# Optimization experiments

Hardware: AMD Instinct MI355X
Metric: run time of the kernel (lower is better)

The kernel has to match this reference:

```python
import jax, jax.numpy as jnp
import numpy as np

NOOBJ_LAMBDA = 0.5
COORD_LAMBDA = 5.0


def _cxcywh_to_xyxy(b):
    cx, cy, w, h = b[..., 0], b[..., 1], b[..., 2], b[..., 3]
    return jnp.stack([cx - w / 2, cy - h / 2, cx + w / 2, cy + h / 2], axis=-1)


def _pairwise_iou(a, b):
    # a: [B, N, 4] xyxy (preds), b: [B, M, 4] xyxy (targets) -> [B, N, M]
    lt = jnp.maximum(a[:, :, None, :2], b[:, None, :, :2])
    rb = jnp.minimum(a[:, :, None, 2:], b[:, None, :, 2:])
    wh = jnp.clip(rb - lt, 0.0)
    inter = wh[..., 0] * wh[..., 1]
    area_a = (a[..., 2] - a[..., 0]) * (a[..., 3] - a[..., 1])
    area_b = (b[..., 2] - b[..., 0]) * (b[..., 3] - b[..., 1])
    union = area_a[:, :, None] + area_b[:, None, :] - inter
    return inter / jnp.where(union > 0, union, 1.0)


def setup_inputs() -> dict:
    key = jax.random.key(0)
    kp, kt, km = jax.random.split(key, 3)
    B = 8192
    # positive values so sqrt(w), sqrt(h) is well-defined (as the torch code assumes)
    pred = jax.random.uniform(kp, (B, 7, 7, 30), dtype=jnp.float32, minval=0.05, maxval=1.0)
    target = jax.random.uniform(kt, (B, 7, 7, 30), dtype=jnp.float32, minval=0.05, maxval=1.0)
    # target confidence channel (index 4) is the obj/noobj indicator: 0 or 1
    obj = (jax.random.uniform(km, (B, 7, 7)) < 0.2).astype(jnp.float32)
    target = target.at[..., 4].set(obj)
    return {"pred_tensor": pred, "target_tensor": target}


def reference(pred_tensor, target_tensor):
    B = pred_tensor.shape[0]
    pred = pred_tensor.reshape(B, 49, 30)
    target = target_tensor.reshape(B, 49, 30)

    conf_t = target[..., 4]            # [B,49]
    noobj = conf_t == 0                # [B,49]
    obj = conf_t > 0                   # [B,49]

    # --- no-object confidence loss (channels 4 and 9) ---
    d4 = pred[..., 4] - target[..., 4]
    d9 = pred[..., 9] - target[..., 9]
    noobj_loss = jnp.sum(jnp.where(noobj, d4 * d4 + d9 * d9, 0.0))

    # --- object cells: 2 boxes per cell, padded to all 49 cells with a mask ---
    pb = pred[..., :10].reshape(B, 98, 5)
    tb = target[..., :10].reshape(B, 98, 5)
    box_mask = jnp.repeat(obj, 2, axis=1)  # [B,98]

    p_xyxy = _cxcywh_to_xyxy(pb[..., :4])
    t_xyxy = _cxcywh_to_xyxy(tb[..., :4])
    iou = _pairwise_iou(p_xyxy, t_xyxy)  # [B,98,98]
    pair_mask = box_mask[:, :, None] & box_mask[:, None, :]
    iou = jnp.where(pair_mask, iou, 0.0)
    max_iou = jnp.max(iou, axis=1)       # max over pred boxes, per target box [B,98]
    cmask = (max_iou != 0) & box_mask    # [B,98]

    cm = cmask.astype(pred.dtype)
    # coord (cx,cy) loss
    dxy = pb[..., :2] - tb[..., :2]
    coord_loss_cxcy = jnp.sum(cm * jnp.sum(dxy * dxy, axis=-1))
    # coord (sqrt w, sqrt h) loss
    dwh = jnp.sqrt(pb[..., 2:4]) - jnp.sqrt(tb[..., 2:4])
    coord_loss_wh = jnp.sum(cm * jnp.sum(dwh * dwh, axis=-1))
    # object confidence loss
    dconf = pb[..., 4] - tb[..., 4]
    obj_loss = jnp.sum(cm * dconf * dconf)

    # --- class loss over object cells ---
    dcls = pred[..., 10:] - target[..., 10:]
    cls_loss = jnp.sum(obj.astype(pred.dtype) * jnp.sum(dcls * dcls, axis=-1))

    bsz = jnp.asarray(B, pred.dtype)
    batch_cls_loss = cls_loss / bsz
    batch_obj_loss = (obj_loss + noobj_loss * NOOBJ_LAMBDA) / bsz
    batch_coord_loss = (coord_loss_cxcy + coord_loss_wh) * COORD_LAMBDA / bsz
    batch_loss = batch_cls_loss + batch_obj_loss + batch_coord_loss
    return (batch_loss, batch_cls_loss, batch_obj_loss, batch_coord_loss)
```

## Files before the change

kernel.cpp:

```cpp
#include <hip/hip_runtime.h>

#define CH 30
#define CELLS 49
#define ROW 1470
#define RPB 4
#define NPAIR 735
#define ITS 12

__device__ __forceinline__ float waveReduce(float v) {
    #pragma unroll
    for (int o = 32; o > 0; o >>= 1) v += __shfl_xor(v, o, 64);
    return v;
}

__global__ __launch_bounds__(256) void yolo_main(const float* __restrict__ pred,
                                                 const float* __restrict__ targ,
                                                 float* __restrict__ ws, int B) {
    const int w = threadIdx.x >> 6;
    const int lane = threadIdx.x & 63;
    const int r = blockIdx.x * RPB + w;
    if (r >= B) return;

    __shared__ float4 boxS[RPB][2 * CELLS];
    __shared__ int clist[RPB][CELLS];

    const float* P = pred + (size_t)r * ROW;
    const float* T = targ + (size_t)r * ROW;
    const float2* P2 = (const float2*)P;
    const float2* T2 = (const float2*)T;

    const int cl = lane < CELLS ? lane : CELLS - 1;
    const float conf = T[cl * CH + 4];

    float2 pv[ITS], tv[ITS];
    #pragma unroll
    for (int it = 0; it < ITS; ++it) {
        const int j = lane + it * 64;
        const int jc = j < NPAIR ? j : NPAIR - 1;
        pv[it] = P2[jc];
        tv[it] = T2[jc];
    }

    const bool isObj = (lane < CELLS) && (conf > 0.f);
    const unsigned long long mask = __ballot(isObj);
    const int nObj = __popcll(mask);
    if (isObj) clist[w][__popcll(mask & ((1ull << lane) - 1ull))] = lane;

    float cls = 0.f, objc = 0.f, coord = 0.f;
    #pragma unroll
    for (int it = 0; it < ITS; ++it) {
        const int j = lane + it * 64;
        const bool valid = j < NPAIR;
        const int cell = (j * 17477) >> 18;
        const int ch0 = 2 * (j - cell * 15);
        const float wobj = (float)((mask >> cell) & 1ull);
        const float dx = pv[it].x - tv[it].x;
        const float dy = pv[it].y - tv[it].y;
        cls += (valid && ch0 >= 10) ? wobj * (dx * dx + dy * dy) : 0.f;
        const float nn = (ch0 == 4 ? dx * dx : 0.f) + (ch0 == 8 ? dy * dy : 0.f);
        objc += valid ? 0.5f * (1.f - wobj) * nn : 0.f;
    }

    const int nBox = 2 * nObj;

    for (int e = lane; e < nBox; e += 64) {
        const int c = clist[w][e >> 1];
        const float* pb = P + c * CH + (e & 1) * 5;
        const float cx = pb[0], cy = pb[1], bw = pb[2], bh = pb[3];
        boxS[w][e] = make_float4(cx - 0.5f * bw, cy - 0.5f * bh,
                                 cx + 0.5f * bw, cy + 0.5f * bh);
    }

    for (int e = lane; e < nBox; e += 64) {
        const int c = clist[w][e >> 1];
        const float* tb = T + c * CH + (e & 1) * 5;
        const float tcx = tb[0], tcy = tb[1], tw = tb[2], th = tb[3];
        const float tx1 = tcx - 0.5f * tw, ty1 = tcy - 0.5f * th;
        const float tx2 = tcx + 0.5f * tw, ty2 = tcy + 0.5f * th;
        const float ta = (tx2 - tx1) * (ty2 - ty1);
        float maxiou = 0.f;
        for (int i = 0; i < nBox; ++i) {
            const float4 pb4 = boxS[w][i];
            const float lx = fmaxf(pb4.x, tx1), ly = fmaxf(pb4.y, ty1);
            const float rx = fminf(pb4.z, tx2), ry = fminf(pb4.w, ty2);
            const float iw = fmaxf(rx - lx, 0.f), ih = fmaxf(ry - ly, 0.f);
            const float inter = iw * ih;
            const float pa = (pb4.z - pb4.x) * (pb4.w - pb4.y);
            const float un = pa + ta - inter;
            const float iou = inter / (un > 0.f ? un : 1.f);
            maxiou = fmaxf(maxiou, iou);
        }
        if (maxiou != 0.f) {
            const float* pb = P + c * CH + (e & 1) * 5;
            const float dcx = pb[0] - tcx, dcy = pb[1] - tcy;
            coord += dcx * dcx + dcy * dcy;
            const float dw = sqrtf(pb[2]) - sqrtf(tw);
            const float dh = sqrtf(pb[3]) - sqrtf(th);
            coord += dw * dw + dh * dh;
            const float dc = pb[4] - tb[4];
            objc += dc * dc;
        }
    }

    cls = waveReduce(cls); objc = waveReduce(objc); coord = waveReduce(coord);
    if (lane == 0) {
        ws[r] = cls;
        ws[B + r] = objc;
        ws[2 * B + r] = coord;
    }
}

__global__ __launch_bounds__(1024) void yolo_reduce(const float* __restrict__ ws,
                                                    float* __restrict__ out,
                                                    int B, float invB) {
    const int tid = threadIdx.x;
    const int w = tid >> 6, lane = tid & 63;
    float c = 0.f, o = 0.f, x = 0.f;
    for (int i = tid; i < B; i += 1024) {
        c += ws[i];
        o += ws[B + i];
        x += ws[2 * B + i];
    }
    c = waveReduce(c); o = waveReduce(o); x = waveReduce(x);
    __shared__ float sred[16][3];
    if (lane == 0) { sred[w][0] = c; sred[w][1] = o; sred[w][2] = x; }
    __syncthreads();
    if (tid == 0) {
        float C = 0.f, O = 0.f, X = 0.f;
        #pragma unroll
        for (int k = 0; k < 16; ++k) { C += sred[k][0]; O += sred[k][1]; X += sred[k][2]; }
        const float bcls = C * invB;
        const float bobj = O * invB;
        const float bcoord = X * 5.0f * invB;
        out[0] = bcls + bobj + bcoord;
        out[1] = bcls;
        out[2] = bobj;
        out[3] = bcoord;
    }
}

extern "C" void kernel_launch(void* const* d_in, const int* in_sizes, int n_in,
                              void* d_out, int out_size, void* d_ws, size_t ws_size,
                              hipStream_t stream) {
    const float* pred = (const float*)d_in[0];
    const float* targ = (const float*)d_in[1];
    float* ws = (float*)d_ws;
    float* out = (float*)d_out;
    const int B = in_sizes[0] / ROW;
    const int NB = (B + RPB - 1) / RPB;

    yolo_main<<<NB, 256, 0, stream>>>(pred, targ, ws, B);
    yolo_reduce<<<1, 1024, 0, stream>>>(ws, out, B, 1.0f / (float)B);
}
```

Before: 122.0 us.

## Process two rows per wave and fuse final reduction via last-block atomic

Each wave now handles two batch rows, issuing the register loads for both rows up front so more memory requests are in flight per wave. The object mask is now built from the already-loaded target registers with a wave OR instead of a separate strided load. Per-block partial sums are combined in shared memory, and the last block to finish, found through an atomic counter, does the final reduction, which removes the second kernel launch. In exchange it doubles register use for the row buffers, adds a memset launch, and adds a thread fence and atomic per block.

```diff
diff --git a/kernel.cpp b/kernel.cpp
--- a/kernel.cpp
+++ b/kernel.cpp
@@ -3,9 +3,10 @@
 #define CH 30
 #define CELLS 49
 #define ROW 1470
-#define RPB 4
 #define NPAIR 735
 #define ITS 12
+#define RPW 2
+#define WPB 4
 
 __device__ __forceinline__ float waveReduce(float v) {
     #pragma unroll
@@ -13,40 +14,30 @@
     return v;
 }
 
-__global__ __launch_bounds__(256) void yolo_main(const float* __restrict__ pred,
-                                                 const float* __restrict__ targ,
-                                                 float* __restrict__ ws, int B) {
-    const int w = threadIdx.x >> 6;
-    const int lane = threadIdx.x & 63;
-    const int r = blockIdx.x * RPB + w;
-    if (r >= B) return;
-
-    __shared__ float4 boxS[RPB][2 * CELLS];
-    __shared__ int clist[RPB][CELLS];
-
-    const float* P = pred + (size_t)r * ROW;
-    const float* T = targ + (size_t)r * ROW;
-    const float2* P2 = (const float2*)P;
-    const float2* T2 = (const float2*)T;
-
-    const int cl = lane < CELLS ? lane : CELLS - 1;
-    const float conf = T[cl * CH + 4];
-
-    float2 pv[ITS], tv[ITS];
+__device__ __forceinline__ unsigned long long waveOr64(unsigned long long m) {
+    #pragma unroll
+    for (int o = 32; o > 0; o >>= 1) m |= __shfl_xor(m, o, 64);
+    return m;
+}
+
+__device__ __forceinline__ void processRow(const float* __restrict__ P,
+                                           const float* __restrict__ T,
+                                           const float2* pv, const float2* tv,
+                                           int lane, float4* boxS, int* clist,
+                                           float& cls, float& objc, float& coord) {
+    unsigned long long contrib = 0ull;
     #pragma unroll
     for (int it = 0; it < ITS; ++it) {
         const int j = lane + it * 64;
-        const int jc = j < NPAIR ? j : NPAIR - 1;
-        pv[it] = P2[jc];
-        tv[it] = T2[jc];
-    }
-
-    const bool isObj = (lane < CELLS) && (conf > 0.f);
-    const unsigned long long mask = __ballot(isObj);
+        const int cell = (j * 17477) >> 18;
+        const int rem = j - cell * 15;
+        if (j < NPAIR && rem == 2 && tv[it].x > 0.f) contrib |= (1ull << cell);
+    }
+    const unsigned long long mask = waveOr64(contrib);
     const int nObj = __popcll(mask);
-    if (isObj) clist[w][__popcll(mask & ((1ull << lane) - 1ull))] = lane;
-
-    float cls = 0.f, objc = 0.f, coord = 0.f;
+    const bool isObj = (lane < CELLS) && ((mask >> lane) & 1ull);
+    if (isObj) clist[__popcll(mask & ((1ull << lane) - 1ull))] = lane;
+
     #pragma unroll
     for (int it = 0; it < ITS; ++it) {
         const int j = lane + it * 64;
@@ -64,15 +55,15 @@
     const int nBox = 2 * nObj;
 
     for (int e = lane; e < nBox; e += 64) {
-        const int c = clist[w][e >> 1];
+        const int c = clist[e >> 1];
         const float* pb = P + c * CH + (e & 1) * 5;
         const float cx = pb[0], cy = pb[1], bw = pb[2], bh = pb[3];
-        boxS[w][e] = make_float4(cx - 0.5f * bw, cy - 0.5f * bh,
-                                 cx + 0.5f * bw, cy + 0.5f * bh);
+        boxS[e] = make_float4(cx - 0.5f * bw, cy - 0.5f * bh,
+                              cx + 0.5f * bw, cy + 0.5f * bh);
     }
 
     for (int e = lane; e < nBox; e += 64) {
-        const int c = clist[w][e >> 1];
+        const int c = clist[e >> 1];
         const float* tb = T + c * CH + (e & 1) * 5;
         const float tcx = tb[0], tcy = tb[1], tw = tb[2], th = tb[3];
         const float tx1 = tcx - 0.5f * tw, ty1 = tcy - 0.5f * th;
@@ -80,7 +71,7 @@
         const float ta = (tx2 - tx1) * (ty2 - ty1);
         float maxiou = 0.f;
         for (int i = 0; i < nBox; ++i) {
-            const float4 pb4 = boxS[w][i];
+            const float4 pb4 = boxS[i];
             const float lx = fmaxf(pb4.x, tx1), ly = fmaxf(pb4.y, ty1);
             const float rx = fminf(pb4.z, tx2), ry = fminf(pb4.w, ty2);
             const float iw = fmaxf(rx - lx, 0.f), ih = fmaxf(ry - ly, 0.f);
@@ -101,41 +92,98 @@
             objc += dc * dc;
         }
     }
+}
+
+__global__ __launch_bounds__(256) void yolo_main(const float* __restrict__ pred,
+                                                 const float* __restrict__ targ,
+                                                 float* __restrict__ ws,
+                                                 int* __restrict__ cnt,
+                                                 float* __restrict__ out,
+                                                 int B, float invB) {
+    const int w = threadIdx.x >> 6;
+    const int lane = threadIdx.x & 63;
+    const int NBLK = gridDim.x;
+    const int r0 = (blockIdx.x * WPB + w) * RPW;
+    const int r1 = r0 + 1;
+    const bool ok0 = r0 < B, ok1 = r1 < B;
+
+    __shared__ float4 boxS[WPB][2 * CELLS];
+    __shared__ int clist[WPB][CELLS];
+    __shared__ float sred[WPB][3];
+    __shared__ int lastFlag;
+
+    const float* P0 = pred + (size_t)r0 * ROW;
+    const float* T0 = targ + (size_t)r0 * ROW;
+    const float* P1 = pred + (size_t)r1 * ROW;
+    const float* T1 = targ + (size_t)r1 * ROW;
+
+    float2 pv0[ITS], tv0[ITS], pv1[ITS], tv1[ITS];
+    if (ok0) {
+        const float2* P2 = (const float2*)P0;
+        const float2* T2 = (const float2*)T0;
+        #pragma unroll
+        for (int it = 0; it < ITS; ++it) {
+            const int j = lane + it * 64;
+            const int jc = j < NPAIR ? j : NPAIR - 1;
+            pv0[it] = P2[jc];
+            tv0[it] = T2[jc];
+        }
+    }
+    if (ok1) {
+        const float2* P2 = (const float2*)P1;
+        const float2* T2 = (const float2*)T1;
+        #pragma unroll
+        for (int it = 0; it < ITS; ++it) {
+            const int j = lane + it * 64;
+            const int jc = j < NPAIR ? j : NPAIR - 1;
+            pv1[it] = P2[jc];
+            tv1[it] = T2[jc];
+        }
+    }
+
+    float cls = 0.f, objc = 0.f, coord = 0.f;
+    if (ok0) processRow(P0, T0, pv0, tv0, lane, boxS[w], clist[w], cls, objc, coord);
+    if (ok1) processRow(P1, T1, pv1, tv1, lane, boxS[w], clist[w], cls, objc, coord);
 
     cls = waveReduce(cls); objc = waveReduce(objc); coord = waveReduce(coord);
-    if (lane == 0) {
-        ws[r] = cls;
-        ws[B + r] = objc;
-        ws[2 * B + r] = coord;
-    }
-}
-
-__global__ __launch_bounds__(1024) void yolo_reduce(const float* __restrict__ ws,
-                                                    float* __restrict__ out,
-                                                    int B, float invB) {
-    const int tid = threadIdx.x;
-    const int w = tid >> 6, lane = tid & 63;
-    float c = 0.f, o = 0.f, x = 0.f;
-    for (int i = tid; i < B; i += 1024) {
-        c += ws[i];
-        o += ws[B + i];
-        x += ws[2 * B + i];
-    }
-    c = waveReduce(c); o = waveReduce(o); x = waveReduce(x);
-    __shared__ float sred[16][3];
-    if (lane == 0) { sred[w][0] = c; sred[w][1] = o; sred[w][2] = x; }
+    if (lane == 0) { sred[w][0] = cls; sred[w][1] = objc; sred[w][2] = coord; }
     __syncthreads();
-    if (tid == 0) {
-        float C = 0.f, O = 0.f, X = 0.f;
+    if (threadIdx.x == 0) {
+        float c = 0.f, o = 0.f, x = 0.f;
         #pragma unroll
-        for (int k = 0; k < 16; ++k) { C += sred[k][0]; O += sred[k][1]; X += sred[k][2]; }
-        const float bcls = C * invB;
-        const float bobj = O * invB;
-        const float bcoord = X * 5.0f * invB;
-        out[0] = bcls + bobj + bcoord;
-        out[1] = bcls;
-        out[2] = bobj;
-        out[3] = bcoord;
+        for (int i = 0; i < WPB; ++i) { c += sred[i][0]; o += sred[i][1]; x += sred[i][2]; }
+        ws[blockIdx.x] = c;
+        ws[NBLK + blockIdx.x] = o;
+        ws[2 * NBLK + blockIdx.x] = x;
+        __threadfence();
+        const int old = atomicAdd(cnt, 1);
+        lastFlag = (old == NBLK - 1) ? 1 : 0;
+    }
+    __syncthreads();
+
+    if (lastFlag) {
+        __threadfence();
+        float c = 0.f, o = 0.f, x = 0.f;
+        for (int i = threadIdx.x; i < NBLK; i += 256) {
+            c += ws[i];
+            o += ws[NBLK + i];
+            x += ws[2 * NBLK + i];
+        }
+        c = waveReduce(c); o = waveReduce(o); x = waveReduce(x);
+        if (lane == 0) { sred[w][0] = c; sred[w][1] = o; sred[w][2] = x; }
+        __syncthreads();
+        if (threadIdx.x == 0) {
+            float C = 0.f, O = 0.f, X = 0.f;
+            #pragma unroll
+            for (int i = 0; i < WPB; ++i) { C += sred[i][0]; O += sred[i][1]; X += sred[i][2]; }
+            const float bcls = C * invB;
+            const float bobj = O * invB;
+            const float bcoord = X * 5.0f * invB;
+            out[0] = bcls + bobj + bcoord;
+            out[1] = bcls;
+            out[2] = bobj;
+            out[3] = bcoord;
+        }
     }
 }
 
@@ -147,8 +195,9 @@
     float* ws = (float*)d_ws;
     float* out = (float*)d_out;
     const int B = in_sizes[0] / ROW;
-    const int NB = (B + RPB - 1) / RPB;
-
-    yolo_main<<<NB, 256, 0, stream>>>(pred, targ, ws, B);
-    yolo_reduce<<<1, 1024, 0, stream>>>(ws, out, B, 1.0f / (float)B);
-}
+    const int NBLK = (B + RPW * WPB - 1) / (RPW * WPB);
+    int* cnt = (int*)(ws + 3 * NBLK);
+
+    hipMemsetAsync(cnt, 0, sizeof(int), stream);
+    yolo_main<<<NBLK, 256, 0, stream>>>(pred, targ, ws, cnt, out, B, 1.0f / (float)B);
+}
```

Result: slower. 158.3 us (+29.7%).

## Split streaming loss and IoU work into separate block roles, fuse final reduction

Applied to the files above, without the earlier changes.

The kernel now uses two kinds of blocks. Some blocks run a flat grid-stride loop over all float2 pairs to compute the class and no-object losses. The other blocks do only the per-row IoU matching. The separate reduction kernel is replaced by a last-block-done pattern: an atomic counter plus threadfence lets the final block sum the per-block partials. This aims to spread the bandwidth-bound streaming work evenly and cut a kernel launch, at the cost of a memset launch, redundant gathers of the conf value per element, and integer divisions in the hot loop.

```diff
diff --git a/kernel.cpp b/kernel.cpp
--- a/kernel.cpp
+++ b/kernel.cpp
@@ -3,9 +3,9 @@
 #define CH 30
 #define CELLS 49
 #define ROW 1470
+#define NPAIR 735u
 #define RPB 4
-#define NPAIR 735
-#define ITS 12
+#define THREADS 256
 
 __device__ __forceinline__ float waveReduce(float v) {
     #pragma unroll
@@ -13,129 +13,134 @@
     return v;
 }
 
-__global__ __launch_bounds__(256) void yolo_main(const float* __restrict__ pred,
-                                                 const float* __restrict__ targ,
-                                                 float* __restrict__ ws, int B) {
+__global__ __launch_bounds__(256, 4) void yolo_fused(const float* __restrict__ pred,
+                                                     const float* __restrict__ targ,
+                                                     float* __restrict__ ws,
+                                                     int* __restrict__ cnt,
+                                                     float* __restrict__ out,
+                                                     int B, int NSb, int NBLK,
+                                                     unsigned total, float invB) {
     const int w = threadIdx.x >> 6;
     const int lane = threadIdx.x & 63;
-    const int r = blockIdx.x * RPB + w;
-    if (r >= B) return;
 
     __shared__ float4 boxS[RPB][2 * CELLS];
     __shared__ int clist[RPB][CELLS];
-
-    const float* P = pred + (size_t)r * ROW;
-    const float* T = targ + (size_t)r * ROW;
-    const float2* P2 = (const float2*)P;
-    const float2* T2 = (const float2*)T;
-
-    const int cl = lane < CELLS ? lane : CELLS - 1;
-    const float conf = T[cl * CH + 4];
-
-    float2 pv[ITS], tv[ITS];
-    #pragma unroll
-    for (int it = 0; it < ITS; ++it) {
-        const int j = lane + it * 64;
-        const int jc = j < NPAIR ? j : NPAIR - 1;
-        pv[it] = P2[jc];
-        tv[it] = T2[jc];
-    }
-
-    const bool isObj = (lane < CELLS) && (conf > 0.f);
-    const unsigned long long mask = __ballot(isObj);
-    const int nObj = __popcll(mask);
-    if (isObj) clist[w][__popcll(mask & ((1ull << lane) - 1ull))] = lane;
+    __shared__ float sred[RPB][3];
+    __shared__ int lastFlag;
 
     float cls = 0.f, objc = 0.f, coord = 0.f;
-    #pragma unroll
-    for (int it = 0; it < ITS; ++it) {
-        const int j = lane + it * 64;
-        const bool valid = j < NPAIR;
-        const int cell = (j * 17477) >> 18;
-        const int ch0 = 2 * (j - cell * 15);
-        const float wobj = (float)((mask >> cell) & 1ull);
-        const float dx = pv[it].x - tv[it].x;
-        const float dy = pv[it].y - tv[it].y;
-        cls += (valid && ch0 >= 10) ? wobj * (dx * dx + dy * dy) : 0.f;
-        const float nn = (ch0 == 4 ? dx * dx : 0.f) + (ch0 == 8 ? dy * dy : 0.f);
-        objc += valid ? 0.5f * (1.f - wobj) * nn : 0.f;
-    }
 
-    const int nBox = 2 * nObj;
+    if ((int)blockIdx.x < NSb) {
+        const float2* p2 = (const float2*)pred;
+        const float2* t2 = (const float2*)targ;
+        const unsigned stride = (unsigned)NSb * THREADS;
+        for (unsigned g = blockIdx.x * THREADS + threadIdx.x; g < total; g += stride) {
+            const float2 p = p2[g];
+            const float2 t = t2[g];
+            const unsigned r = g / NPAIR;
+            const unsigned j = g - r * NPAIR;
+            const unsigned cell = j / 15u;
+            const unsigned ch0 = 2u * (j - cell * 15u);
+            const float conf = targ[(size_t)r * ROW + cell * CH + 4];
+            const float wobj = conf > 0.f ? 1.f : 0.f;
+            const float dx = p.x - t.x;
+            const float dy = p.y - t.y;
+            cls += (ch0 >= 10u) ? wobj * (dx * dx + dy * dy) : 0.f;
+            const float nn = (ch0 == 4u ? dx * dx : 0.f) + (ch0 == 8u ? dy * dy : 0.f);
+            objc += 0.5f * (1.f - wobj) * nn;
+        }
+    } else {
+        const int r = ((int)blockIdx.x - NSb) * RPB + w;
+        if (r < B) {
+            const float* P = pred + (size_t)r * ROW;
+            const float* T = targ + (size_t)r * ROW;
 
-    for (int e = lane; e < nBox; e += 64) {
-        const int c = clist[w][e >> 1];
-        const float* pb = P + c * CH + (e & 1) * 5;
-        const float cx = pb[0], cy = pb[1], bw = pb[2], bh = pb[3];
-        boxS[w][e] = make_float4(cx - 0.5f * bw, cy - 0.5f * bh,
-                                 cx + 0.5f * bw, cy + 0.5f * bh);
-    }
+            const bool isObj = (lane < CELLS) && (T[lane * CH + 4] > 0.f);
+            const unsigned long long mask = __ballot(isObj);
+            const int nObj = __popcll(mask);
+            if (isObj) clist[w][__popcll(mask & ((1ull << lane) - 1ull))] = lane;
+            const int nBox = 2 * nObj;
 
-    for (int e = lane; e < nBox; e += 64) {
-        const int c = clist[w][e >> 1];
-        const float* tb = T + c * CH + (e & 1) * 5;
-        const float tcx = tb[0], tcy = tb[1], tw = tb[2], th = tb[3];
-        const float tx1 = tcx - 0.5f * tw, ty1 = tcy - 0.5f * th;
-        const float tx2 = tcx + 0.5f * tw, ty2 = tcy + 0.5f * th;
-        const float ta = (tx2 - tx1) * (ty2 - ty1);
-        float maxiou = 0.f;
-        for (int i = 0; i < nBox; ++i) {
-            const float4 pb4 = boxS[w][i];
-            const float lx = fmaxf(pb4.x, tx1), ly = fmaxf(pb4.y, ty1);
-            const float rx = fminf(pb4.z, tx2), ry = fminf(pb4.w, ty2);
-            const float iw = fmaxf(rx - lx, 0.f), ih = fmaxf(ry - ly, 0.f);
-            const float inter = iw * ih;
-            const float pa = (pb4.z - pb4.x) * (pb4.w - pb4.y);
-            const float un = pa + ta - inter;
-            const float iou = inter / (un > 0.f ? un : 1.f);
-            maxiou = fmaxf(maxiou, iou);
-        }
-        if (maxiou != 0.f) {
-            const float* pb = P + c * CH + (e & 1) * 5;
-            const float dcx = pb[0] - tcx, dcy = pb[1] - tcy;
-            coord += dcx * dcx + dcy * dcy;
-            const float dw = sqrtf(pb[2]) - sqrtf(tw);
-            const float dh = sqrtf(pb[3]) - sqrtf(th);
-            coord += dw * dw + dh * dh;
-            const float dc = pb[4] - tb[4];
-            objc += dc * dc;
+            for (int e = lane; e < nBox; e += 64) {
+                const int c = clist[w][e >> 1];
+                const float* pb = P + c * CH + (e & 1) * 5;
+                const float cx = pb[0], cy = pb[1], bw = pb[2], bh = pb[3];
+                boxS[w][e] = make_float4(cx - 0.5f * bw, cy - 0.5f * bh,
+                                         cx + 0.5f * bw, cy + 0.5f * bh);
+            }
+
+            for (int e = lane; e < nBox; e += 64) {
+                const int c = clist[w][e >> 1];
+                const float* tb = T + c * CH + (e & 1) * 5;
+                const float* pb = P + c * CH + (e & 1) * 5;
+                const float tcx = tb[0], tcy = tb[1], tw = tb[2], th = tb[3];
+                const float tx1 = tcx - 0.5f * tw, ty1 = tcy - 0.5f * th;
+                const float tx2 = tcx + 0.5f * tw, ty2 = tcy + 0.5f * th;
+                const float ta = (tx2 - tx1) * (ty2 - ty1);
+                float maxiou = 0.f;
+                for (int i = 0; i < nBox; ++i) {
+                    const float4 b4 = boxS[w][i];
+                    const float lx = fmaxf(b4.x, tx1), ly = fmaxf(b4.y, ty1);
+                    const float rx = fminf(b4.z, tx2), ry = fminf(b4.w, ty2);
+                    const float iw = fmaxf(rx - lx, 0.f), ih = fmaxf(ry - ly, 0.f);
+                    const float inter = iw * ih;
+                    const float pa = (b4.z - b4.x) * (b4.w - b4.y);
+                    const float un = pa + ta - inter;
+                    const float iou = inter / (un > 0.f ? un : 1.f);
+                    maxiou = fmaxf(maxiou, iou);
+                }
+                if (maxiou != 0.f) {
+                    const float dcx = pb[0] - tcx, dcy = pb[1] - tcy;
+                    coord += dcx * dcx + dcy * dcy;
+                    const float dw = sqrtf(pb[2]) - sqrtf(tw);
+                    const float dh = sqrtf(pb[3]) - sqrtf(th);
+                    coord += dw * dw + dh * dh;
+                    const float dc = pb[4] - tb[4];
+                    objc += dc * dc;
+                }
+            }
         }
     }
 
     cls = waveReduce(cls); objc = waveReduce(objc); coord = waveReduce(coord);
-    if (lane == 0) {
-        ws[r] = cls;
-        ws[B + r] = objc;
-        ws[2 * B + r] = coord;
+    if (lane == 0) { sred[w][0] = cls; sred[w][1] = objc; sred[w][2] = coord; }
+    __syncthreads();
+    if (threadIdx.x == 0) {
+        float c = 0.f, o = 0.f, x = 0.f;
+        #pragma unroll
+        for (int i = 0; i < RPB; ++i) { c += sred[i][0]; o += sred[i][1]; x += sred[i][2]; }
+        ws[blockIdx.x] = c;
+        ws[NBLK + blockIdx.x] = o;
+        ws[2 * NBLK + blockIdx.x] = x;
+        __threadfence();
+        const int old = atomicAdd(cnt, 1);
+        lastFlag = (old == NBLK - 1) ? 1 : 0;
     }
-}
+    __syncthreads();
 
-__global__ __launch_bounds__(1024) void yolo_reduce(const float* __restrict__ ws,
-                                                    float* __restrict__ out,
-                                                    int B, float invB) {
-    const int tid = threadIdx.x;
-    const int w = tid >> 6, lane = tid & 63;
-    float c = 0.f, o = 0.f, x = 0.f;
-    for (int i = tid; i < B; i += 1024) {
-        c += ws[i];
-        o += ws[B + i];
-        x += ws[2 * B + i];
-    }
-    c = waveReduce(c); o = waveReduce(o); x = waveReduce(x);
-    __shared__ float sred[16][3];
-    if (lane == 0) { sred[w][0] = c; sred[w][1] = o; sred[w][2] = x; }
-    __syncthreads();
-    if (tid == 0) {
-        float C = 0.f, O = 0.f, X = 0.f;
-        #pragma unroll
-        for (int k = 0; k < 16; ++k) { C += sred[k][0]; O += sred[k][1]; X += sred[k][2]; }
-        const float bcls = C * invB;
-        const float bobj = O * invB;
-        const float bcoord = X * 5.0f * invB;
-        out[0] = bcls + bobj + bcoord;
-        out[1] = bcls;
-        out[2] = bobj;
-        out[3] = bcoord;
+    if (lastFlag) {
+        __threadfence();
+        float c = 0.f, o = 0.f, x = 0.f;
+        for (int i = threadIdx.x; i < NBLK; i += THREADS) {
+            c += ws[i];
+            o += ws[NBLK + i];
+            x += ws[2 * NBLK + i];
+        }
+        c = waveReduce(c); o = waveReduce(o); x = waveReduce(x);
+        if (lane == 0) { sred[w][0] = c; sred[w][1] = o; sred[w][2] = x; }
+        __syncthreads();
+        if (threadIdx.x == 0) {
+            float C = 0.f, O = 0.f, X = 0.f;
+            #pragma unroll
+            for (int i = 0; i < RPB; ++i) { C += sred[i][0]; O += sred[i][1]; X += sred[i][2]; }
+            const float bcls = C * invB;
+            const float bobj = O * invB;
+            const float bcoord = X * 5.0f * invB;
+            out[0] = bcls + bobj + bcoord;
+            out[1] = bcls;
+            out[2] = bobj;
+            out[3] = bcoord;
+        }
     }
 }
 
@@ -147,8 +152,13 @@
     float* ws = (float*)d_ws;
     float* out = (float*)d_out;
     const int B = in_sizes[0] / ROW;
-    const int NB = (B + RPB - 1) / RPB;
+    const int NR = (B + RPB - 1) / RPB;
+    const int NS = 2 * NR;
+    const int NBLK = NS + NR;
+    const unsigned total = (unsigned)B * NPAIR;
+    int* cnt = (int*)(ws + 3 * NBLK);
 
-    yolo_main<<<NB, 256, 0, stream>>>(pred, targ, ws, B);
-    yolo_reduce<<<1, 1024, 0, stream>>>(ws, out, B, 1.0f / (float)B);
+    hipMemsetAsync(cnt, 0, sizeof(int), stream);
+    yolo_fused<<<NBLK, THREADS, 0, stream>>>(pred, targ, ws, cnt, out,
+                                             B, NS, NBLK, total, 1.0f / (float)B);
 }
```

Result: slower. 323.2 us (+164.8%).

## Process two rows per wave with float4 loads and software-pipelined prefetch

Applied to the files above, without the earlier changes.

Each wave now handles two consecutive rows, treating them as one contiguous span read with float4 loads. It uses a rotating register buffer that prefetches later slots while earlier ones are computed. Blocks shrink to 128 threads and reduce per-block partials in shared memory, so the final reduce pass reads fewer workspace entries. The cost is a per-element div/mod to recover cell and channel, more register pressure, and a serial IoU phase over both rows.

```diff
diff --git a/kernel.cpp b/kernel.cpp
--- a/kernel.cpp
+++ b/kernel.cpp
@@ -3,9 +3,10 @@
 #define CH 30
 #define CELLS 49
 #define ROW 1470
-#define RPB 4
-#define NPAIR 735
-#define ITS 12
+#define NF4 735
+#define SLOTS 12
+#define DEPTH 6
+#define THREADS 128
 
 __device__ __forceinline__ float waveReduce(float v) {
     #pragma unroll
@@ -13,85 +14,44 @@
     return v;
 }
 
-__global__ __launch_bounds__(256) void yolo_main(const float* __restrict__ pred,
-                                                 const float* __restrict__ targ,
-                                                 float* __restrict__ ws, int B) {
-    const int w = threadIdx.x >> 6;
-    const int lane = threadIdx.x & 63;
-    const int r = blockIdx.x * RPB + w;
-    if (r >= B) return;
-
-    __shared__ float4 boxS[RPB][2 * CELLS];
-    __shared__ int clist[RPB][CELLS];
-
-    const float* P = pred + (size_t)r * ROW;
-    const float* T = targ + (size_t)r * ROW;
-    const float2* P2 = (const float2*)P;
-    const float2* T2 = (const float2*)T;
-
-    const int cl = lane < CELLS ? lane : CELLS - 1;
-    const float conf = T[cl * CH + 4];
-
-    float2 pv[ITS], tv[ITS];
-    #pragma unroll
-    for (int it = 0; it < ITS; ++it) {
-        const int j = lane + it * 64;
-        const int jc = j < NPAIR ? j : NPAIR - 1;
-        pv[it] = P2[jc];
-        tv[it] = T2[jc];
-    }
-
-    const bool isObj = (lane < CELLS) && (conf > 0.f);
-    const unsigned long long mask = __ballot(isObj);
+__device__ __forceinline__ void boxRow(const float* __restrict__ P,
+                                       const float* __restrict__ T,
+                                       unsigned long long mask, int lane,
+                                       float4* boxS, int* clist,
+                                       float& objc, float& coord) {
     const int nObj = __popcll(mask);
-    if (isObj) clist[w][__popcll(mask & ((1ull << lane) - 1ull))] = lane;
-
-    float cls = 0.f, objc = 0.f, coord = 0.f;
-    #pragma unroll
-    for (int it = 0; it < ITS; ++it) {
-        const int j = lane + it * 64;
-        const bool valid = j < NPAIR;
-        const int cell = (j * 17477) >> 18;
-        const int ch0 = 2 * (j - cell * 15);
-        const float wobj = (float)((mask >> cell) & 1ull);
-        const float dx = pv[it].x - tv[it].x;
-        const float dy = pv[it].y - tv[it].y;
-        cls += (valid && ch0 >= 10) ? wobj * (dx * dx + dy * dy) : 0.f;
-        const float nn = (ch0 == 4 ? dx * dx : 0.f) + (ch0 == 8 ? dy * dy : 0.f);
-        objc += valid ? 0.5f * (1.f - wobj) * nn : 0.f;
-    }
-
+    const bool isObj = (lane < CELLS) && ((mask >> lane) & 1ull);
+    if (isObj) clist[__popcll(mask & ((1ull << lane) - 1ull))] = lane;
     const int nBox = 2 * nObj;
 
     for (int e = lane; e < nBox; e += 64) {
-        const int c = clist[w][e >> 1];
+        const int c = clist[e >> 1];
         const float* pb = P + c * CH + (e & 1) * 5;
         const float cx = pb[0], cy = pb[1], bw = pb[2], bh = pb[3];
-        boxS[w][e] = make_float4(cx - 0.5f * bw, cy - 0.5f * bh,
-                                 cx + 0.5f * bw, cy + 0.5f * bh);
-    }
-
+        boxS[e] = make_float4(cx - 0.5f * bw, cy - 0.5f * bh,
+                              cx + 0.5f * bw, cy + 0.5f * bh);
+    }
     for (int e = lane; e < nBox; e += 64) {
-        const int c = clist[w][e >> 1];
+        const int c = clist[e >> 1];
         const float* tb = T + c * CH + (e & 1) * 5;
+        const float* pb = P + c * CH + (e & 1) * 5;
         const float tcx = tb[0], tcy = tb[1], tw = tb[2], th = tb[3];
         const float tx1 = tcx - 0.5f * tw, ty1 = tcy - 0.5f * th;
         const float tx2 = tcx + 0.5f * tw, ty2 = tcy + 0.5f * th;
         const float ta = (tx2 - tx1) * (ty2 - ty1);
         float maxiou = 0.f;
         for (int i = 0; i < nBox; ++i) {
-            const float4 pb4 = boxS[w][i];
-            const float lx = fmaxf(pb4.x, tx1), ly = fmaxf(pb4.y, ty1);
-            const float rx = fminf(pb4.z, tx2), ry = fminf(pb4.w, ty2);
+            const float4 b4 = boxS[i];
+            const float lx = fmaxf(b4.x, tx1), ly = fmaxf(b4.y, ty1);
+            const float rx = fminf(b4.z, tx2), ry = fminf(b4.w, ty2);
             const float iw = fmaxf(rx - lx, 0.f), ih = fmaxf(ry - ly, 0.f);
             const float inter = iw * ih;
-            const float pa = (pb4.z - pb4.x) * (pb4.w - pb4.y);
+            const float pa = (b4.z - b4.x) * (b4.w - b4.y);
             const float un = pa + ta - inter;
             const float iou = inter / (un > 0.f ? un : 1.f);
             maxiou = fmaxf(maxiou, iou);
         }
         if (maxiou != 0.f) {
-            const float* pb = P + c * CH + (e & 1) * 5;
             const float dcx = pb[0] - tcx, dcy = pb[1] - tcy;
             coord += dcx * dcx + dcy * dcy;
             const float dw = sqrtf(pb[2]) - sqrtf(tw);
@@ -101,25 +61,126 @@
             objc += dc * dc;
         }
     }
+}
+
+__global__ __launch_bounds__(THREADS) void yolo_main(const float* __restrict__ pred,
+                                                     const float* __restrict__ targ,
+                                                     float* __restrict__ ws, int B) {
+    const int w = threadIdx.x >> 6;
+    const int lane = threadIdx.x & 63;
+    const int waveId = blockIdx.x * 2 + w;
+    const int r0 = waveId * 2, r1 = r0 + 1;
+    const bool ok0 = r0 < B, ok1 = r1 < B;
+
+    __shared__ float4 boxS[2][2 * CELLS];
+    __shared__ int clist[2][CELLS];
+    __shared__ float sred[2][3];
+
+    float cls = 0.f, objc = 0.f, coord = 0.f;
+    unsigned long long mask0 = 0ull, mask1 = 0ull;
+
+    const float* P0 = pred + (size_t)r0 * ROW;
+    const float* T0 = targ + (size_t)r0 * ROW;
+    const float* P1 = P0 + ROW;
+    const float* T1 = T0 + ROW;
+
+    if (ok0 && ok1) {
+        const int cl = lane < CELLS ? lane : CELLS - 1;
+        const float c0 = T0[cl * CH + 4];
+        const float c1 = T1[cl * CH + 4];
+
+        const float4* P4 = (const float4*)P0;
+        const float4* T4 = (const float4*)T0;
+
+        float4 pv[DEPTH], tv[DEPTH];
+        #pragma unroll
+        for (int i = 0; i < DEPTH; ++i) {
+            const int f = lane + i * 64;
+            const int fc = f < NF4 ? f : NF4 - 1;
+            pv[i] = P4[fc];
+            tv[i] = T4[fc];
+        }
+
+        mask0 = __ballot((lane < CELLS) && (c0 > 0.f));
+        mask1 = __ballot((lane < CELLS) && (c1 > 0.f));
+
+        #pragma unroll
+        for (int i = 0; i < SLOTS; ++i) {
+            if (i + DEPTH < SLOTS) {
+                const int f = lane + (i + DEPTH) * 64;
+                const int fc = f < NF4 ? f : NF4 - 1;
+            }
+            const float4 p = pv[i % DEPTH];
+            const float4 t = tv[i % DEPTH];
+            if (i + DEPTH < SLOTS) {
+                const int f = lane + (i + DEPTH) * 64;
+                const int fc = f < NF4 ? f : NF4 - 1;
+                pv[i % DEPTH] = P4[fc];
+                tv[i % DEPTH] = T4[fc];
+            }
+            const int f = lane + i * 64;
+            const bool valid = f < NF4;
+            const float pe[4] = {p.x, p.y, p.z, p.w};
+            const float te[4] = {t.x, t.y, t.z, t.w};
+            #pragma unroll
+            for (int k = 0; k < 4; ++k) {
+                const unsigned j2 = 4u * (unsigned)f + (unsigned)k;
+                const unsigned s = j2 >= (unsigned)ROW;
+                const unsigned j = j2 - s * (unsigned)ROW;
+                const unsigned cell = j / 30u;
+                const unsigned ch = j - cell * 30u;
+                const unsigned long long m = s ? mask1 : mask0;
+                const float wobj = (float)((m >> cell) & 1ull);
+                const float d = pe[k] - te[k];
+                const float d2 = d * d;
+                cls += (valid && ch >= 10u) ? wobj * d2 : 0.f;
+                const float nn = (ch == 4u || ch == 9u) ? d2 : 0.f;
+                objc += valid ? 0.5f * (1.f - wobj) * nn : 0.f;
+            }
+        }
+
+        boxRow(P0, T0, mask0, lane, boxS[w], clist[w], objc, coord);
+        boxRow(P1, T1, mask1, lane, boxS[w], clist[w], objc, coord);
+    } else if (ok0) {
+        const int cl = lane < CELLS ? lane : CELLS - 1;
+        mask0 = __ballot((lane < CELLS) && (T0[cl * CH + 4] > 0.f));
+        const float2* P2 = (const float2*)P0;
+        const float2* T2 = (const float2*)T0;
+        for (int j = lane; j < ROW / 2; j += 64) {
+            const float2 p = P2[j];
+            const float2 t = T2[j];
+            const unsigned cell = (unsigned)j / 15u;
+            const unsigned ch0 = 2u * ((unsigned)j - cell * 15u);
+            const float wobj = (float)((mask0 >> cell) & 1ull);
+            const float dx = p.x - t.x, dy = p.y - t.y;
+            cls += (ch0 >= 10u) ? wobj * (dx * dx + dy * dy) : 0.f;
+            const float nn = (ch0 == 4u ? dx * dx : 0.f) + (ch0 == 8u ? dy * dy : 0.f);
+            objc += 0.5f * (1.f - wobj) * nn;
+        }
+        boxRow(P0, T0, mask0, lane, boxS[w], clist[w], objc, coord);
+    }
 
     cls = waveReduce(cls); objc = waveReduce(objc); coord = waveReduce(coord);
-    if (lane == 0) {
-        ws[r] = cls;
-        ws[B + r] = objc;
-        ws[2 * B + r] = coord;
+    if (lane == 0) { sred[w][0] = cls; sred[w][1] = objc; sred[w][2] = coord; }
+    __syncthreads();
+    if (threadIdx.x == 0) {
+        const int NBLK = gridDim.x;
+        ws[blockIdx.x]            = sred[0][0] + sred[1][0];
+        ws[NBLK + blockIdx.x]     = sred[0][1] + sred[1][1];
+        ws[2 * NBLK + blockIdx.x] = sred[0][2] + sred[1][2];
     }
 }
 
 __global__ __launch_bounds__(1024) void yolo_reduce(const float* __restrict__ ws,
                                                     float* __restrict__ out,
-                                                    int B, float invB) {
+                                                    int NBLK, float invB) {
     const int tid = threadIdx.x;
     const int w = tid >> 6, lane = tid & 63;
     float c = 0.f, o = 0.f, x = 0.f;
-    for (int i = tid; i < B; i += 1024) {
+    for (int i = tid; i < NBLK; i += 1024) {
         c += ws[i];
-        o += ws[B + i];
-        x += ws[2 * B + i];
+        o += ws[NBLK + i];
+        x += ws[2 * NBLK + i];
     }
     c = waveReduce(c); o = waveReduce(o); x = waveReduce(x);
     __shared__ float sred[16][3];
@@ -147,8 +208,8 @@
     float* ws = (float*)d_ws;
     float* out = (float*)d_out;
     const int B = in_sizes[0] / ROW;
-    const int NB = (B + RPB - 1) / RPB;
-
-    yolo_main<<<NB, 256, 0, stream>>>(pred, targ, ws, B);
-    yolo_reduce<<<1, 1024, 0, stream>>>(ws, out, B, 1.0f / (float)B);
-}
+    const int NBLK = (B + 3) / 4;
+
+    yolo_main<<<NBLK, THREADS, 0, stream>>>(pred, targ, ws, B);
+    yolo_reduce<<<1, 1024, 0, stream>>>(ws, out, NBLK, 1.0f / (float)B);
+}
```

Result: slower. 135.5 us (+11.0%).
